# Kernel optimization log

Hardware: AMD Instinct MI355X
Metric: run time of the kernel (lower is better)

The kernel has to match this reference:

```python
import jax, jax.numpy as jnp
import numpy as np

B, S, D = 4, 2048, 1024
LAYERS = 2
NLOPS = 4
GAMMA = 0.01          # lindblad_gamma
COND_TH = 100.0       # condition_threshold
EPS = 1e-6


def setup_inputs() -> dict:
    key = jax.random.key(0)
    ks = jax.random.split(key, 9)
    x_real = jax.random.normal(ks[0], (B, S, D), jnp.float32)
    x_imag = jax.random.normal(ks[1], (B, S, D), jnp.float32)
    H_prev = jax.random.uniform(ks[2], (B, D, D), jnp.float32)
    eye = jnp.eye(D, dtype=jnp.float32)
    # base mixing layer (stand-in for ComplexMamba3Layer): near-identity complex linear
    W_real = eye[None, :, :] + 0.02 * jax.random.normal(ks[3], (LAYERS, D, D), jnp.float32)
    W_imag = 0.02 * jax.random.normal(ks[4], (LAYERS, D, D), jnp.float32)
    L_ops = 0.5 * jax.random.normal(ks[5], (LAYERS, NLOPS, D), jnp.float32)
    theta = jax.random.uniform(ks[6], (LAYERS,), jnp.float32, 0.0, 0.5)
    jump_scale = 0.9 * jnp.ones((LAYERS,), jnp.float32)
    kappa_th = 0.1 * jnp.ones((LAYERS,), jnp.float32)   # curvature_threshold per layer
    return dict(x_real=x_real, x_imag=x_imag, H_prev=H_prev,
                W_real=W_real, W_imag=W_imag, L_ops=L_ops,
                theta=theta, jump_scale=jump_scale, kappa_th=kappa_th)


def _v8_forward(x_real, x_imag, H_prev, W_real, W_imag, L_ops, theta, jump_scale, kappa_th):
    psi = jax.lax.complex(x_real, x_imag)  # [B,S,D] complex64
    Hp = H_prev                            # [B,D,D] real (prev Hamiltonian, detached)
    for l in range(LAYERS):
        residual = psi
        # --- base layer: complex linear mix ---
        Wc = jax.lax.complex(W_real[l], W_imag[l])
        out = jnp.einsum('bsd,de->bse', psi, Wc)
        branch_delta = out - residual
        # --- delta-RMS normalize (no_grad -> stop_gradient) ---
        rms = jnp.sqrt(jnp.clip(jnp.mean(branch_delta.real ** 2 + branch_delta.imag ** 2), 1e-12, None))
        rms = jax.lax.stop_gradient(jnp.maximum(rms, 1e-3))
        b = branch_delta / rms
        # --- Lindblad dissipation: diagonal damping gamma * sum_k L_k^2 ---
        damp = GAMMA * jnp.sum(L_ops[l] ** 2, axis=0)  # [D]
        b = b * (1.0 - damp)
        # --- approximate Hamiltonian H = (1/S) sum_s |psi_s><psi_s| (no_grad) ---
        mag = jnp.abs(b)                                # [B,S,D]
        H = jax.lax.stop_gradient(jnp.einsum('bsd,bse->bde', mag, mag) / S)  # [B,D,D]
        # --- hybrid automata: curvature K = ||H - Hp||_F / ||Hp||_F ---
        diff_n = jnp.sqrt(jnp.sum((H - Hp) ** 2, axis=(1, 2)))
        prev_n = jnp.sqrt(jnp.sum(Hp ** 2, axis=(1, 2)))
        K = diff_n / (prev_n + EPS)                     # [B]
        jumped = K > kappa_th[l]
        b = jnp.where(jumped[:, None, None], b * jump_scale[l].astype(jnp.complex64), b)
        Hp = H
        # --- quaternionic escape: diag-based condition estimate, phase rotation ---
        dg = jnp.diagonal(H, axis1=1, axis2=2)          # [B,D]
        cond = jnp.max(dg, axis=1) / (jnp.min(dg, axis=1) + 1e-12)
        escaped = cond > COND_TH
        rot = jnp.exp(1j * theta[l]).astype(jnp.complex64)
        b = jnp.where(escaped[:, None, None], b * rot, b)
        # --- rescale and residual ---
        b = b * rms
        psi = residual + b
    return jnp.stack([psi.real, psi.imag], axis=0)  # [2,B,S,D] float32


def reference(x_real, x_imag, H_prev, W_real, W_imag, L_ops, theta, jump_scale, kappa_th):
    return _v8_forward(x_real, x_imag, H_prev, W_real, W_imag, L_ops, theta, jump_scale, kappa_th)
```

## Files before the change

kernel.cpp:

```cpp
#include <hip/hip_runtime.h>

#define B_ 4
#define S_ 2048
#define D_ 1024
#define M_ (B_*S_)
#define K2_ 2048
#define N2_ 2048
#define NTOT (B_*S_*D_)
#define DD (D_*D_)

typedef __attribute__((ext_vector_type(4))) float f32x4;
typedef __attribute__((ext_vector_type(8))) short short8;
typedef __attribute__((ext_vector_type(4))) unsigned short u16x4;
typedef __attribute__((ext_vector_type(8))) unsigned short u16x8;

static __device__ __forceinline__ unsigned short f2bf(float f) {
    union { float f; unsigned int u; } v; v.f = f;
    unsigned int u = v.u;
    unsigned int r = (u + 0x7fffu + ((u >> 16) & 1u)) >> 16;
    return (unsigned short)r;
}
static __device__ __forceinline__ float bf2f(unsigned short h) {
    union { unsigned int u; float f; } v; v.u = ((unsigned int)h) << 16;
    return v.f;
}


__global__ __launch_bounds__(256, 2) void gemm_main2(const unsigned short* __restrict__ A2,
                                                     const unsigned short* __restrict__ B2T,
                                                     unsigned short* __restrict__ bd2,
                                                     unsigned short* __restrict__ magT,
                                                     float* __restrict__ scal, int l)
{
    __shared__ unsigned short smem[3 * 128 * 64];
    __shared__ float red[4];
    unsigned short* As  = smem;
    unsigned short* Bsr = smem + 8192;
    unsigned short* Bsi = smem + 16384;

    f32x4 accr[4][4], acci[4][4];
#pragma unroll
    for (int i = 0; i < 4; ++i)
#pragma unroll
        for (int j = 0; j < 4; ++j) { accr[i][j] = (f32x4)0.0f; acci[i][j] = (f32x4)0.0f; }

    const int nt = blockIdx.x, mt = blockIdx.y;
    const int tid = threadIdx.x, wave = tid >> 6, lane = tid & 63;
    const int q = lane >> 4, lm = lane & 15;
    const int wm = (wave >> 1) * 64, wn = (wave & 1) * 64;
    const int crow = lane >> 3;
    const int gcol = ((lane & 7) ^ crow) * 8;

    const unsigned short* Ag  = A2  + (long)mt * 128 * K2_;
    const unsigned short* Bgr = B2T + (long)(nt * 128) * K2_;
    const unsigned short* Bgi = B2T + (long)(nt * 128 + 1024) * K2_;

    for (int kt = 0; kt < K2_ / 64; ++kt) {
        const long k0 = (long)kt * 64;
        __syncthreads();
#pragma unroll
        for (int i2 = 0; i2 < 4; ++i2) {
            int c   = i2 * 4 + wave;
            int row = c * 8 + crow;
            long go = (long)row * K2_ + k0 + gcol;
            __builtin_amdgcn_global_load_lds((const __attribute__((address_space(1))) void*)(Ag + go),
                                             (__attribute__((address_space(3))) void*)(As + c * 512), 16, 0, 0);
            __builtin_amdgcn_global_load_lds((const __attribute__((address_space(1))) void*)(Bgr + go),
                                             (__attribute__((address_space(3))) void*)(Bsr + c * 512), 16, 0, 0);
            __builtin_amdgcn_global_load_lds((const __attribute__((address_space(1))) void*)(Bgi + go),
                                             (__attribute__((address_space(3))) void*)(Bsi + c * 512), 16, 0, 0);
        }
        __syncthreads();
#pragma unroll
        for (int kk = 0; kk < 64; kk += 32) {
            short8 a[4], br[4], bi[4];
#pragma unroll
            for (int t = 0; t < 4; ++t) {
                int arow  = wm + t * 16 + lm;
                int aslot = ((kk >> 3) + q) ^ (arow & 7);
                a[t] = *(const short8*)(As + arow * 64 + aslot * 8);
                int brow  = wn + t * 16 + lm;
                int bslot = ((kk >> 3) + q) ^ (brow & 7);
                br[t] = *(const short8*)(Bsr + brow * 64 + bslot * 8);
                bi[t] = *(const short8*)(Bsi + brow * 64 + bslot * 8);
            }
#pragma unroll
            for (int um = 0; um < 4; ++um)
#pragma unroll
                for (int un = 0; un < 4; ++un) {
                    accr[um][un] = __builtin_amdgcn_mfma_f32_16x16x32_bf16(a[um], br[un], accr[um][un], 0, 0, 0);
                    acci[um][un] = __builtin_amdgcn_mfma_f32_16x16x32_bf16(a[um], bi[un], acci[um][un], 0, 0, 0);
                }
        }
    }

    __syncthreads();
    unsigned short* magLds = smem;
    float ss = 0.f;
#pragma unroll
    for (int um = 0; um < 4; ++um) {
#pragma unroll
        for (int un = 0; un < 4; ++un) {
            int colb = wn + un * 16 + lm;
            int coln = nt * 128 + colb;
            u16x4 magv;
#pragma unroll
            for (int i = 0; i < 4; ++i) {
                long rowm = (long)mt * 128 + wm + um * 16 + q * 4 + i;
                float vr = accr[um][un][i];
                float vi = acci[um][un][i];
                bd2[rowm * N2_ + coln]        = f2bf(vr);
                bd2[rowm * N2_ + 1024 + coln] = f2bf(vi);
                float s2 = vr * vr + vi * vi;
                ss += s2;
                magv[i] = f2bf(sqrtf(s2));
            }
            *(u16x4*)(magLds + colb * 136 + wm + um * 16 + q * 4) = magv;
        }
    }
    for (int off = 32; off > 0; off >>= 1) ss += __shfl_down(ss, off);
    if (lane == 0) red[wave] = ss;
    __syncthreads();
    if (tid == 0) atomicAdd(scal + l, red[0] + red[1] + red[2] + red[3]);

    const int b   = mt >> 4;
    const long s0 = (long)(mt & 15) * 128;
#pragma unroll
    for (int it = 0; it < 8; ++it) {
        int sid = it * 256 + tid;
        int row = sid >> 4, seg = sid & 15;
        unsigned short* dst = magT + (long)b * D_ * S_ + (long)(nt * 128 + row) * S_ + s0 + seg * 8;
        *(u16x8*)dst = *(const u16x8*)(magLds + row * 136 + seg * 8);
    }
}

__device__ __forceinline__ void mfma_gemm_64(const unsigned short* __restrict__ Ag, long astride,
                                             const unsigned short* __restrict__ Bg, long bstride,
                                             int kiters,
                                             unsigned short* As, unsigned short* Bs,
                                             f32x4 acc[2][2])
{
    const int tid  = threadIdx.x;
    const int wave = tid >> 6, lane = tid & 63;
    const int q    = lane >> 4, lm = lane & 15;
    const int wm   = (wave >> 1) * 32, wn = (wave & 1) * 32;
    const int crow = lane >> 3;
    const int gcol = ((lane & 7) ^ crow) * 8;

    for (int kt = 0; kt < kiters; ++kt) {
        const long k0 = (long)kt * 64;
        __syncthreads();
#pragma unroll
        for (int i2 = 0; i2 < 2; ++i2) {
            int c   = i2 * 4 + wave;
            int row = c * 8 + crow;
            const unsigned short* ga = Ag + (long)row * astride + k0 + gcol;
            const unsigned short* gb = Bg + (long)row * bstride + k0 + gcol;
            __builtin_amdgcn_global_load_lds((const __attribute__((address_space(1))) void*)ga,
                                             (__attribute__((address_space(3))) void*)(As + c * 512), 16, 0, 0);
            __builtin_amdgcn_global_load_lds((const __attribute__((address_space(1))) void*)gb,
                                             (__attribute__((address_space(3))) void*)(Bs + c * 512), 16, 0, 0);
        }
        __syncthreads();
#pragma unroll
        for (int kk = 0; kk < 64; kk += 32) {
            short8 a[2], b[2];
#pragma unroll
            for (int t = 0; t < 2; ++t) {
                int arow  = wm + t * 16 + lm;
                int aslot = ((kk >> 3) + q) ^ (arow & 7);
                a[t] = *(const short8*)(As + arow * 64 + aslot * 8);
                int brow  = wn + t * 16 + lm;
                int bslot = ((kk >> 3) + q) ^ (brow & 7);
                b[t] = *(const short8*)(Bs + brow * 64 + bslot * 8);
            }
#pragma unroll
            for (int um = 0; um < 2; ++um)
#pragma unroll
                for (int un = 0; un < 2; ++un)
                    acc[um][un] = __builtin_amdgcn_mfma_f32_16x16x32_bf16(a[um], b[un], acc[um][un], 0, 0, 0);
        }
    }
}

__global__ __launch_bounds__(256) void gemm_H(const unsigned short* __restrict__ magT,
                                              const float* __restrict__ Hp,
                                              float* __restrict__ H,
                                              float* __restrict__ scal,
                                              const float* __restrict__ dampv, int l)
{
    __shared__ unsigned short As[64 * 64];
    __shared__ unsigned short Bs[64 * 64];
    __shared__ float redd[4], redp[4];

    int idx = blockIdx.x, ty = 0;
    while (idx >= 16 - ty) { idx -= 16 - ty; ++ty; }
    const int tx = ty + idx;
    const int b = blockIdx.y;
    const int diag = (tx == ty);

    f32x4 acc[2][2];
#pragma unroll
    for (int i = 0; i < 2; ++i)
#pragma unroll
        for (int j = 0; j < 2; ++j) acc[i][j] = (f32x4)0.0f;

    const unsigned short* Mb = magT + (long)b * D_ * S_;
    mfma_gemm_64(Mb + (long)ty * 64 * S_, S_,
                 Mb + (long)tx * 64 * S_, S_, S_ / 64, As, Bs, acc);

    float mean = fmaxf(scal[l] / (float)NTOT, 1e-12f);
    float inv  = 1.0f / fmaxf(sqrtf(mean), 1e-3f);
    const float scale = inv * inv / (float)S_;

    const int tid = threadIdx.x, wave = tid >> 6, lane = tid & 63;
    const int q = lane >> 4, lm = lane & 15;
    const int wm = (wave >> 1) * 32, wn = (wave & 1) * 32;
    float d2 = 0.f, p2 = 0.f;
#pragma unroll
    for (int um = 0; um < 2; ++um) {
#pragma unroll
        for (int un = 0; un < 2; ++un) {
            int coln = tx * 64 + wn + un * 16 + lm;
            float de = dampv[coln];
#pragma unroll
            for (int i = 0; i < 4; ++i) {
                int rowm = ty * 64 + wm + um * 16 + q * 4 + i;
                float h = acc[um][un][i] * scale * dampv[rowm] * de;
                long adr = (long)b * DD + (long)rowm * D_ + coln;
                float hp1 = Hp[adr];
                float df1 = h - hp1;
                if (diag) {
                    H[adr] = h;
                    d2 += df1 * df1;
                    p2 += hp1 * hp1;
                    if (rowm == coln) {
                        atomicMax((int*)scal + 18 + l * 4 + b, __float_as_int(h));
                        atomicMin((int*)scal + 26 + l * 4 + b, __float_as_int(h));
                    }
                } else {
                    long adrT = (long)b * DD + (long)coln * D_ + rowm;
                    float hp2 = Hp[adrT];
                    H[adr]  = h;
                    H[adrT] = h;
                    float df2 = h - hp2;
                    d2 += df1 * df1 + df2 * df2;
                    p2 += hp1 * hp1 + hp2 * hp2;
                }
            }
        }
    }
    for (int off = 32; off > 0; off >>= 1) { d2 += __shfl_down(d2, off); p2 += __shfl_down(p2, off); }
    if (lane == 0) { redd[wave] = d2; redp[wave] = p2; }
    __syncthreads();
    if (tid == 0) {
        atomicAdd(scal + 2 + l * 4 + b,  redd[0] + redd[1] + redd[2] + redd[3]);
        atomicAdd(scal + 10 + l * 4 + b, redp[0] + redp[1] + redp[2] + redp[3]);
    }
}

__global__ void init_kernel(const float* __restrict__ xr, const float* __restrict__ xi,
                            float* __restrict__ psi_r, float* __restrict__ psi_i,
                            unsigned short* __restrict__ A2, float* __restrict__ scal)
{
    if (blockIdx.x == 0 && threadIdx.x < 34)
        scal[threadIdx.x] = (threadIdx.x >= 26) ? 3.402823466e38f : 0.0f;
    long t = (long)blockIdx.x * 256 + threadIdx.x;
    long i = t * 4;
    f32x4 r  = *(const f32x4*)(xr + i);
    f32x4 im = *(const f32x4*)(xi + i);
    *(f32x4*)(psi_r + i) = r;
    *(f32x4*)(psi_i + i) = im;
    long m = i / D_; int d = (int)(i % D_);
    u16x4 rr, ii;
#pragma unroll
    for (int j = 0; j < 4; ++j) { rr[j] = f2bf(r[j]); ii[j] = f2bf(im[j]); }
    *(u16x4*)(A2 + m * K2_ + d) = rr;
    *(u16x4*)(A2 + m * K2_ + D_ + d) = ii;
}

__global__ __launch_bounds__(256) void pack_b2t(const float* __restrict__ Wr_all,
                                                const float* __restrict__ Wi_all,
                                                unsigned short* __restrict__ B2T, int l)
{
    __shared__ float T[64][65];
    const float* Wr = Wr_all + (long)l * DD;
    const float* Wi = Wi_all + (long)l * DD;
    int k0 = blockIdx.x * 64;
    int n0 = blockIdx.y * 64;
    int t = threadIdx.x;
#pragma unroll
    for (int it = 0; it < 16; ++it) {
        int idx = it * 256 + t;
        int kl = idx >> 6, nl = idx & 63;
        int k = k0 + kl, n = n0 + nl;
        float v;
        if (k < D_) v = (n < D_) ? Wr[k * D_ + n] : Wi[k * D_ + (n - D_)];
        else        v = (n < D_) ? -Wi[(k - D_) * D_ + n] : Wr[(k - D_) * D_ + (n - D_)];
        if (k == n) v -= 1.0f;
        T[kl][nl] = v;
    }
    __syncthreads();
#pragma unroll
    for (int it = 0; it < 16; ++it) {
        int idx = it * 256 + t;
        int nl = idx >> 6, kl = idx & 63;
        B2T[(long)(n0 + nl) * K2_ + (k0 + kl)] = f2bf(T[kl][nl]);
    }
}

__global__ void damp_kernel(const float* __restrict__ Lops, float* __restrict__ dampv)
{
    int g = blockIdx.x;
    int l = g >> 2;
    int d = (g & 3) * 256 + threadIdx.x;
    const float* Lp = Lops + (long)l * 4 * D_;
    float s = 0.f;
#pragma unroll
    for (int k = 0; k < 4; ++k) { float v = Lp[k * D_ + d]; s += v * v; }
    dampv[l * D_ + d] = 1.0f - 0.01f * s;
}

__global__ void update_kernel(const unsigned short* __restrict__ bd2,
                              const float* __restrict__ dampv,
                              const float* __restrict__ scal,
                              const float* __restrict__ theta,
                              const float* __restrict__ jscale,
                              const float* __restrict__ kappa, int l,
                              float* __restrict__ psi_r,
                              float* __restrict__ psi_i,
                              unsigned short* __restrict__ A2,
                              int write_a2)
{
    long t = (long)blockIdx.x * 256 + threadIdx.x;
    long i = t * 4;
    long m = i / D_; int d = (int)(i % D_);
    int b = (int)(m >> 11);

    float dn = sqrtf(scal[2 + l * 4 + b]);
    float pn = sqrtf(scal[10 + l * 4 + b]);
    float K  = dn / (pn + 1e-6f);
    float mx = __int_as_float(((const int*)scal)[18 + l * 4 + b]);
    float mn = __int_as_float(((const int*)scal)[26 + l * 4 + b]);
    int jumped  = K > kappa[l];
    int escaped = (mx / (mn + 1e-12f)) > 100.0f;
    float js = jumped ? jscale[l] : 1.0f;
    float th = theta[l];
    float fr = js * (escaped ? cosf(th) : 1.0f);
    float fi = js * (escaped ? sinf(th) : 0.0f);

    u16x4 brv = *(const u16x4*)(bd2 + m * N2_ + d);
    u16x4 biv = *(const u16x4*)(bd2 + m * N2_ + D_ + d);
    f32x4 w  = *(const f32x4*)(dampv + d);
    f32x4 pr = *(const f32x4*)(psi_r + i);
    f32x4 pi = *(const f32x4*)(psi_i + i);
    u16x4 ar, ai;
#pragma unroll
    for (int j = 0; j < 4; ++j) {
        float br = bf2f(brv[j]) * w[j];
        float bi = bf2f(biv[j]) * w[j];
        float nr = pr[j] + br * fr - bi * fi;
        float ni = pi[j] + br * fi + bi * fr;
        pr[j] = nr; pi[j] = ni;
        ar[j] = f2bf(nr); ai[j] = f2bf(ni);
    }
    *(f32x4*)(psi_r + i) = pr;
    *(f32x4*)(psi_i + i) = pi;
    if (write_a2) {
        *(u16x4*)(A2 + m * K2_ + d) = ar;
        *(u16x4*)(A2 + m * K2_ + D_ + d) = ai;
    }
}

extern "C" void kernel_launch(void* const* d_in, const int* in_sizes, int n_in,
                              void* d_out, int out_size, void* d_ws, size_t ws_size,
                              hipStream_t stream)
{
    const float* xr     = (const float*)d_in[0];
    const float* xi     = (const float*)d_in[1];
    const float* Hprev  = (const float*)d_in[2];
    const float* Wr     = (const float*)d_in[3];
    const float* Wi     = (const float*)d_in[4];
    const float* Lops   = (const float*)d_in[5];
    const float* theta  = (const float*)d_in[6];
    const float* jscale = (const float*)d_in[7];
    const float* kappa  = (const float*)d_in[8];

    float* psi_r = (float*)d_out;
    float* psi_i = psi_r + NTOT;

    char* ws = (char*)d_ws;
    unsigned short* A2   = (unsigned short*)ws;
    unsigned short* B2T  = (unsigned short*)(ws + 33554432);
    unsigned short* bd2  = (unsigned short*)(ws + 41943040);
    unsigned short* magT = (unsigned short*)(ws + 75497472);
    float* H             = (float*)(ws + 92274688);
    float* scal          = (float*)(ws + 109051904);
    float* dampv         = scal + 64;

    init_kernel<<<NTOT / 4 / 256, 256, 0, stream>>>(xr, xi, psi_r, psi_i, A2, scal);
    damp_kernel<<<8, 256, 0, stream>>>(Lops, dampv);

    for (int l = 0; l < 2; ++l) {
        const float* Hp = (l == 0) ? Hprev : H;
        pack_b2t<<<dim3(32, 32), 256, 0, stream>>>(Wr, Wi, B2T, l);
        gemm_main2<<<dim3(8, M_ / 128), 256, 0, stream>>>(A2, B2T, bd2, magT, scal, l);
        gemm_H<<<dim3(136, B_), 256, 0, stream>>>(magT, Hp, H, scal, dampv + l * D_, l);
        update_kernel<<<NTOT / 4 / 256, 256, 0, stream>>>(
            bd2, dampv + l * D_, scal, theta, jscale, kappa, l,
            psi_r, psi_i, A2, l == 0);
    }
}
```

Before: 457.5 us.

## Split-K the Hamiltonian GEMM with 128x128 tiles plus separate reduce kernel

After: 487.5 us. 6.6% more time.

```diff
diff --git a/kernel.cpp b/kernel.cpp
--- a/kernel.cpp
+++ b/kernel.cpp
@@ -134,16 +134,16 @@
     }
 }
 
-__device__ __forceinline__ void mfma_gemm_64(const unsigned short* __restrict__ Ag, long astride,
-                                             const unsigned short* __restrict__ Bg, long bstride,
-                                             int kiters,
-                                             unsigned short* As, unsigned short* Bs,
-                                             f32x4 acc[2][2])
+__device__ __forceinline__ void mfma_gemm_128(const unsigned short* __restrict__ Ag, long astride,
+                                              const unsigned short* __restrict__ Bg, long bstride,
+                                              int kiters,
+                                              unsigned short* As, unsigned short* Bs,
+                                              f32x4 acc[4][4])
 {
     const int tid  = threadIdx.x;
     const int wave = tid >> 6, lane = tid & 63;
     const int q    = lane >> 4, lm = lane & 15;
-    const int wm   = (wave >> 1) * 32, wn = (wave & 1) * 32;
+    const int wm   = (wave >> 1) * 64, wn = (wave & 1) * 64;
     const int crow = lane >> 3;
     const int gcol = ((lane & 7) ^ crow) * 8;
 
@@ -151,7 +151,7 @@
         const long k0 = (long)kt * 64;
         __syncthreads();
 #pragma unroll
-        for (int i2 = 0; i2 < 2; ++i2) {
+        for (int i2 = 0; i2 < 4; ++i2) {
             int c   = i2 * 4 + wave;
             int row = c * 8 + crow;
             const unsigned short* ga = Ag + (long)row * astride + k0 + gcol;
@@ -164,9 +164,9 @@
         __syncthreads();
 #pragma unroll
         for (int kk = 0; kk < 64; kk += 32) {
-            short8 a[2], b[2];
-#pragma unroll
-            for (int t = 0; t < 2; ++t) {
+            short8 a[4], b[4];
+#pragma unroll
+            for (int t = 0; t < 4; ++t) {
                 int arow  = wm + t * 16 + lm;
                 int aslot = ((kk >> 3) + q) ^ (arow & 7);
                 a[t] = *(const short8*)(As + arow * 64 + aslot * 8);
@@ -175,83 +175,109 @@
                 b[t] = *(const short8*)(Bs + brow * 64 + bslot * 8);
             }
 #pragma unroll
-            for (int um = 0; um < 2; ++um)
-#pragma unroll
-                for (int un = 0; un < 2; ++un)
+            for (int um = 0; um < 4; ++um)
+#pragma unroll
+                for (int un = 0; un < 4; ++un)
                     acc[um][un] = __builtin_amdgcn_mfma_f32_16x16x32_bf16(a[um], b[un], acc[um][un], 0, 0, 0);
         }
     }
 }
 
-__global__ __launch_bounds__(256) void gemm_H(const unsigned short* __restrict__ magT,
-                                              const float* __restrict__ Hp,
-                                              float* __restrict__ H,
-                                              float* __restrict__ scal,
-                                              const float* __restrict__ dampv, int l)
-{
-    __shared__ unsigned short As[64 * 64];
-    __shared__ unsigned short Bs[64 * 64];
+__global__ __launch_bounds__(256, 2) void gemmH_split(const unsigned short* __restrict__ magT,
+                                                      float* __restrict__ pbuf)
+{
+    __shared__ unsigned short As[128 * 64];
+    __shared__ unsigned short Bs[128 * 64];
+    f32x4 acc[4][4];
+#pragma unroll
+    for (int i = 0; i < 4; ++i)
+#pragma unroll
+        for (int j = 0; j < 4; ++j) acc[i][j] = (f32x4)0.0f;
+
+    const int pair = blockIdx.x, b = blockIdx.y, kc = blockIdx.z;
+    int idx = pair, ty = 0;
+    while (idx >= 8 - ty) { idx -= 8 - ty; ++ty; }
+    const int tx = ty + idx;
+
+    const unsigned short* Mb = magT + (long)b * D_ * S_ + (long)kc * 512;
+    mfma_gemm_128(Mb + (long)ty * 128 * S_, S_,
+                  Mb + (long)tx * 128 * S_, S_, 8, As, Bs, acc);
+
+    float* pt = pbuf + ((long)(kc * 36 + pair) * B_ + b) * 16384;
+    const int tid = threadIdx.x, wave = tid >> 6, lane = tid & 63;
+    const int q = lane >> 4, lm = lane & 15;
+    const int wm = (wave >> 1) * 64, wn = (wave & 1) * 64;
+#pragma unroll
+    for (int um = 0; um < 4; ++um)
+#pragma unroll
+        for (int un = 0; un < 4; ++un) {
+            int c = wn + un * 16 + lm;
+#pragma unroll
+            for (int i = 0; i < 4; ++i) {
+                int r = wm + um * 16 + q * 4 + i;
+                pt[r * 128 + c] = acc[um][un][i];
+            }
+        }
+}
+
+__global__ __launch_bounds__(256) void reduce_H(const float* __restrict__ pbuf,
+                                                const float* __restrict__ Hp,
+                                                float* __restrict__ H,
+                                                float* __restrict__ scal,
+                                                const float* __restrict__ dampv, int l)
+{
     __shared__ float redd[4], redp[4];
-
-    int idx = blockIdx.x, ty = 0;
-    while (idx >= 16 - ty) { idx -= 16 - ty; ++ty; }
-    const int tx = ty + idx;
-    const int b = blockIdx.y;
-    const int diag = (tx == ty);
-
-    f32x4 acc[2][2];
-#pragma unroll
-    for (int i = 0; i < 2; ++i)
-#pragma unroll
-        for (int j = 0; j < 2; ++j) acc[i][j] = (f32x4)0.0f;
-
-    const unsigned short* Mb = magT + (long)b * D_ * S_;
-    mfma_gemm_64(Mb + (long)ty * 64 * S_, S_,
-                 Mb + (long)tx * 64 * S_, S_, S_ / 64, As, Bs, acc);
+    const int pair = blockIdx.x, b = blockIdx.y;
+    int idx0 = pair, ty = 0;
+    while (idx0 >= 8 - ty) { idx0 -= 8 - ty; ++ty; }
+    const int tx = ty + idx0;
+    const int diag_tile = (tx == ty);
 
     float mean = fmaxf(scal[l] / (float)NTOT, 1e-12f);
     float inv  = 1.0f / fmaxf(sqrtf(mean), 1e-3f);
     const float scale = inv * inv / (float)S_;
 
-    const int tid = threadIdx.x, wave = tid >> 6, lane = tid & 63;
-    const int q = lane >> 4, lm = lane & 15;
-    const int wm = (wave >> 1) * 32, wn = (wave & 1) * 32;
+    const int tid = threadIdx.x;
     float d2 = 0.f, p2 = 0.f;
-#pragma unroll
-    for (int um = 0; um < 2; ++um) {
-#pragma unroll
-        for (int un = 0; un < 2; ++un) {
-            int coln = tx * 64 + wn + un * 16 + lm;
-            float de = dampv[coln];
-#pragma unroll
-            for (int i = 0; i < 4; ++i) {
-                int rowm = ty * 64 + wm + um * 16 + q * 4 + i;
-                float h = acc[um][un][i] * scale * dampv[rowm] * de;
-                long adr = (long)b * DD + (long)rowm * D_ + coln;
-                float hp1 = Hp[adr];
-                float df1 = h - hp1;
-                if (diag) {
-                    H[adr] = h;
-                    d2 += df1 * df1;
-                    p2 += hp1 * hp1;
-                    if (rowm == coln) {
-                        atomicMax((int*)scal + 18 + l * 4 + b, __float_as_int(h));
-                        atomicMin((int*)scal + 26 + l * 4 + b, __float_as_int(h));
-                    }
-                } else {
-                    long adrT = (long)b * DD + (long)coln * D_ + rowm;
-                    float hp2 = Hp[adrT];
-                    H[adr]  = h;
-                    H[adrT] = h;
-                    float df2 = h - hp2;
-                    d2 += df1 * df1 + df2 * df2;
-                    p2 += hp1 * hp1 + hp2 * hp2;
-                }
+    float dmx = 0.f, dmn = 3.402823466e38f;
+    for (int it = 0; it < 64; ++it) {
+        int idx = it * 256 + tid;
+        int r = idx >> 7, c = idx & 127;
+        int gr = ty * 128 + r, gc = tx * 128 + c;
+        float s = pbuf[((long)(0 * 36 + pair) * B_ + b) * 16384 + idx]
+                + pbuf[((long)(1 * 36 + pair) * B_ + b) * 16384 + idx]
+                + pbuf[((long)(2 * 36 + pair) * B_ + b) * 16384 + idx]
+                + pbuf[((long)(3 * 36 + pair) * B_ + b) * 16384 + idx];
+        float h = s * scale * dampv[gr] * dampv[gc];
+        long adr = (long)b * DD + (long)gr * D_ + gc;
+        if (l == 0) {
+            float hp1 = Hp[adr];
+            H[adr] = h;
+            float df1 = h - hp1;
+            if (diag_tile) {
+                d2 += df1 * df1; p2 += hp1 * hp1;
+            } else {
+                float hp2 = Hp[(long)b * DD + (long)gc * D_ + gr];
+                float df2 = h - hp2;
+                d2 += df1 * df1 + df2 * df2;
+                p2 += hp1 * hp1 + hp2 * hp2;
             }
-        }
-    }
+        } else {
+            float hp1 = Hp[adr];
+            float df1 = h - hp1;
+            float w = diag_tile ? 1.0f : 2.0f;
+            d2 += w * df1 * df1;
+            p2 += w * hp1 * hp1;
+        }
+        if (diag_tile && gr == gc) { dmx = fmaxf(dmx, h); dmn = fminf(dmn, h); }
+    }
+    int lane = tid & 63, wave = tid >> 6;
     for (int off = 32; off > 0; off >>= 1) { d2 += __shfl_down(d2, off); p2 += __shfl_down(p2, off); }
     if (lane == 0) { redd[wave] = d2; redp[wave] = p2; }
+    if (diag_tile) {
+        atomicMax((int*)scal + 18 + l * 4 + b, __float_as_int(dmx));
+        atomicMin((int*)scal + 26 + l * 4 + b, __float_as_int(dmn));
+    }
     __syncthreads();
     if (tid == 0) {
         atomicAdd(scal + 2 + l * 4 + b,  redd[0] + redd[1] + redd[2] + redd[3]);
@@ -260,7 +286,6 @@
 }
 
 __global__ void init_kernel(const float* __restrict__ xr, const float* __restrict__ xi,
-                            float* __restrict__ psi_r, float* __restrict__ psi_i,
                             unsigned short* __restrict__ A2, float* __restrict__ scal)
 {
     if (blockIdx.x == 0 && threadIdx.x < 34)
@@ -269,8 +294,6 @@
     long i = t * 4;
     f32x4 r  = *(const f32x4*)(xr + i);
     f32x4 im = *(const f32x4*)(xi + i);
-    *(f32x4*)(psi_r + i) = r;
-    *(f32x4*)(psi_i + i) = im;
     long m = i / D_; int d = (int)(i % D_);
     u16x4 rr, ii;
 #pragma unroll
@@ -327,8 +350,10 @@
                               const float* __restrict__ theta,
                               const float* __restrict__ jscale,
                               const float* __restrict__ kappa, int l,
-                              float* __restrict__ psi_r,
-                              float* __restrict__ psi_i,
+                              const float* __restrict__ src_r,
+                              const float* __restrict__ src_i,
+                              float* __restrict__ dst_r,
+                              float* __restrict__ dst_i,
                               unsigned short* __restrict__ A2,
                               int write_a2)
 {
@@ -352,8 +377,8 @@
     u16x4 brv = *(const u16x4*)(bd2 + m * N2_ + d);
     u16x4 biv = *(const u16x4*)(bd2 + m * N2_ + D_ + d);
     f32x4 w  = *(const f32x4*)(dampv + d);
-    f32x4 pr = *(const f32x4*)(psi_r + i);
-    f32x4 pi = *(const f32x4*)(psi_i + i);
+    f32x4 pr = *(const f32x4*)(src_r + i);
+    f32x4 pi = *(const f32x4*)(src_i + i);
     u16x4 ar, ai;
 #pragma unroll
     for (int j = 0; j < 4; ++j) {
@@ -364,8 +389,8 @@
         pr[j] = nr; pi[j] = ni;
         ar[j] = f2bf(nr); ai[j] = f2bf(ni);
     }
-    *(f32x4*)(psi_r + i) = pr;
-    *(f32x4*)(psi_i + i) = pi;
+    *(f32x4*)(dst_r + i) = pr;
+    *(f32x4*)(dst_i + i) = pi;
     if (write_a2) {
         *(u16x4*)(A2 + m * K2_ + d) = ar;
         *(u16x4*)(A2 + m * K2_ + D_ + d) = ai;
@@ -391,6 +416,7 @@
 
     char* ws = (char*)d_ws;
     unsigned short* A2   = (unsigned short*)ws;
+    float* pbuf          = (float*)ws;
     unsigned short* B2T  = (unsigned short*)(ws + 33554432);
     unsigned short* bd2  = (unsigned short*)(ws + 41943040);
     unsigned short* magT = (unsigned short*)(ws + 75497472);
@@ -398,16 +424,18 @@
     float* scal          = (float*)(ws + 109051904);
     float* dampv         = scal + 64;
 
-    init_kernel<<<NTOT / 4 / 256, 256, 0, stream>>>(xr, xi, psi_r, psi_i, A2, scal);
+    init_kernel<<<NTOT / 4 / 256, 256, 0, stream>>>(xr, xi, A2, scal);
     damp_kernel<<<8, 256, 0, stream>>>(Lops, dampv);
 
     for (int l = 0; l < 2; ++l) {
-        const float* Hp = (l == 0) ? Hprev : H;
         pack_b2t<<<dim3(32, 32), 256, 0, stream>>>(Wr, Wi, B2T, l);
         gemm_main2<<<dim3(8, M_ / 128), 256, 0, stream>>>(A2, B2T, bd2, magT, scal, l);
-        gemm_H<<<dim3(136, B_), 256, 0, stream>>>(magT, Hp, H, scal, dampv + l * D_, l);
+        gemmH_split<<<dim3(36, B_, 4), 256, 0, stream>>>(magT, pbuf);
+        reduce_H<<<dim3(36, B_), 256, 0, stream>>>(
+            pbuf, (l == 0) ? Hprev : H, H, scal, dampv + l * D_, l);
         update_kernel<<<NTOT / 4 / 256, 256, 0, stream>>>(
             bd2, dampv + l * D_, scal, theta, jscale, kappa, l,
+            (l == 0) ? xr : psi_r, (l == 0) ? xi : psi_i,
             psi_r, psi_i, A2, l == 0);
     }
 }
```

## Trim psi and H traffic, widen gemm_H K-step, and reduce diagonal atomics

Applied to the files above, without the earlier changes.

Result: faster. 427.9 us (-6.5%).

```diff
diff --git a/kernel.cpp b/kernel.cpp
--- a/kernel.cpp
+++ b/kernel.cpp
@@ -134,89 +134,85 @@
     }
 }
 
-__device__ __forceinline__ void mfma_gemm_64(const unsigned short* __restrict__ Ag, long astride,
-                                             const unsigned short* __restrict__ Bg, long bstride,
-                                             int kiters,
-                                             unsigned short* As, unsigned short* Bs,
-                                             f32x4 acc[2][2])
-{
-    const int tid  = threadIdx.x;
-    const int wave = tid >> 6, lane = tid & 63;
-    const int q    = lane >> 4, lm = lane & 15;
-    const int wm   = (wave >> 1) * 32, wn = (wave & 1) * 32;
+__global__ __launch_bounds__(256, 4) void gemm_H(const unsigned short* __restrict__ magT,
+                                                 const float* __restrict__ Hp,
+                                                 float* __restrict__ H,
+                                                 float* __restrict__ scal,
+                                                 const float* __restrict__ dampv, int l)
+{
+    __shared__ unsigned short As[2 * 64 * 64];
+    __shared__ unsigned short Bs[2 * 64 * 64];
+    __shared__ float redd[4], redp[4];
+
+    const int slot = blockIdx.x;
+    const int b = slot & 3;
+    int pair = (slot >> 2) * 68 + blockIdx.y;
+    int idx = pair, ty = 0;
+    while (idx >= 16 - ty) { idx -= 16 - ty; ++ty; }
+    const int tx = ty + idx;
+    const int diag = (tx == ty);
+
+    f32x4 acc[2][2];
+#pragma unroll
+    for (int i = 0; i < 2; ++i)
+#pragma unroll
+        for (int j = 0; j < 2; ++j) acc[i][j] = (f32x4)0.0f;
+
+    const int tid = threadIdx.x, wave = tid >> 6, lane = tid & 63;
+    const int q = lane >> 4, lm = lane & 15;
+    const int wm = (wave >> 1) * 32, wn = (wave & 1) * 32;
     const int crow = lane >> 3;
     const int gcol = ((lane & 7) ^ crow) * 8;
 
-    for (int kt = 0; kt < kiters; ++kt) {
-        const long k0 = (long)kt * 64;
+    const unsigned short* Ag = magT + (long)b * D_ * S_ + (long)ty * 64 * S_;
+    const unsigned short* Bg = magT + (long)b * D_ * S_ + (long)tx * 64 * S_;
+
+    for (int kt = 0; kt < 16; ++kt) {
+        const long k0 = (long)kt * 128;
         __syncthreads();
 #pragma unroll
-        for (int i2 = 0; i2 < 2; ++i2) {
-            int c   = i2 * 4 + wave;
-            int row = c * 8 + crow;
-            const unsigned short* ga = Ag + (long)row * astride + k0 + gcol;
-            const unsigned short* gb = Bg + (long)row * bstride + k0 + gcol;
-            __builtin_amdgcn_global_load_lds((const __attribute__((address_space(1))) void*)ga,
-                                             (__attribute__((address_space(3))) void*)(As + c * 512), 16, 0, 0);
-            __builtin_amdgcn_global_load_lds((const __attribute__((address_space(1))) void*)gb,
-                                             (__attribute__((address_space(3))) void*)(Bs + c * 512), 16, 0, 0);
+        for (int p = 0; p < 2; ++p) {
+#pragma unroll
+            for (int i2 = 0; i2 < 2; ++i2) {
+                int c   = i2 * 4 + wave;
+                int row = c * 8 + crow;
+                long go = (long)row * S_ + k0 + p * 64 + gcol;
+                __builtin_amdgcn_global_load_lds((const __attribute__((address_space(1))) void*)(Ag + go),
+                                                 (__attribute__((address_space(3))) void*)(As + p * 4096 + c * 512), 16, 0, 0);
+                __builtin_amdgcn_global_load_lds((const __attribute__((address_space(1))) void*)(Bg + go),
+                                                 (__attribute__((address_space(3))) void*)(Bs + p * 4096 + c * 512), 16, 0, 0);
+            }
         }
         __syncthreads();
 #pragma unroll
-        for (int kk = 0; kk < 64; kk += 32) {
-            short8 a[2], b[2];
-#pragma unroll
-            for (int t = 0; t < 2; ++t) {
-                int arow  = wm + t * 16 + lm;
-                int aslot = ((kk >> 3) + q) ^ (arow & 7);
-                a[t] = *(const short8*)(As + arow * 64 + aslot * 8);
-                int brow  = wn + t * 16 + lm;
-                int bslot = ((kk >> 3) + q) ^ (brow & 7);
-                b[t] = *(const short8*)(Bs + brow * 64 + bslot * 8);
+        for (int p = 0; p < 2; ++p) {
+#pragma unroll
+            for (int kk = 0; kk < 64; kk += 32) {
+                short8 a[2], bb[2];
+#pragma unroll
+                for (int t = 0; t < 2; ++t) {
+                    int arow  = wm + t * 16 + lm;
+                    int aslot = ((kk >> 3) + q) ^ (arow & 7);
+                    a[t] = *(const short8*)(As + p * 4096 + arow * 64 + aslot * 8);
+                    int brow  = wn + t * 16 + lm;
+                    int bslot = ((kk >> 3) + q) ^ (brow & 7);
+                    bb[t] = *(const short8*)(Bs + p * 4096 + brow * 64 + bslot * 8);
+                }
+#pragma unroll
+                for (int um = 0; um < 2; ++um)
+#pragma unroll
+                    for (int un = 0; un < 2; ++un)
+                        acc[um][un] = __builtin_amdgcn_mfma_f32_16x16x32_bf16(a[um], bb[un], acc[um][un], 0, 0, 0);
             }
-#pragma unroll
-            for (int um = 0; um < 2; ++um)
-#pragma unroll
-                for (int un = 0; un < 2; ++un)
-                    acc[um][un] = __builtin_amdgcn_mfma_f32_16x16x32_bf16(a[um], b[un], acc[um][un], 0, 0, 0);
-        }
-    }
-}
-
-__global__ __launch_bounds__(256) void gemm_H(const unsigned short* __restrict__ magT,
-                                              const float* __restrict__ Hp,
-                                              float* __restrict__ H,
-                                              float* __restrict__ scal,
-                                              const float* __restrict__ dampv, int l)
-{
-    __shared__ unsigned short As[64 * 64];
-    __shared__ unsigned short Bs[64 * 64];
-    __shared__ float redd[4], redp[4];
-
-    int idx = blockIdx.x, ty = 0;
-    while (idx >= 16 - ty) { idx -= 16 - ty; ++ty; }
-    const int tx = ty + idx;
-    const int b = blockIdx.y;
-    const int diag = (tx == ty);
-
-    f32x4 acc[2][2];
-#pragma unroll
-    for (int i = 0; i < 2; ++i)
-#pragma unroll
-        for (int j = 0; j < 2; ++j) acc[i][j] = (f32x4)0.0f;
-
-    const unsigned short* Mb = magT + (long)b * D_ * S_;
-    mfma_gemm_64(Mb + (long)ty * 64 * S_, S_,
-                 Mb + (long)tx * 64 * S_, S_, S_ / 64, As, Bs, acc);
+        }
+    }
 
     float mean = fmaxf(scal[l] / (float)NTOT, 1e-12f);
     float inv  = 1.0f / fmaxf(sqrtf(mean), 1e-3f);
     const float scale = inv * inv / (float)S_;
 
-    const int tid = threadIdx.x, wave = tid >> 6, lane = tid & 63;
-    const int q = lane >> 4, lm = lane & 15;
-    const int wm = (wave >> 1) * 32, wn = (wave & 1) * 32;
     float d2 = 0.f, p2 = 0.f;
+    float dmx = 0.f, dmn = 3.402823466e38f;
 #pragma unroll
     for (int um = 0; um < 2; ++um) {
 #pragma unroll
@@ -231,18 +227,14 @@
                 float hp1 = Hp[adr];
                 float df1 = h - hp1;
                 if (diag) {
-                    H[adr] = h;
+                    if (l == 0) H[adr] = h;
                     d2 += df1 * df1;
                     p2 += hp1 * hp1;
-                    if (rowm == coln) {
-                        atomicMax((int*)scal + 18 + l * 4 + b, __float_as_int(h));
-                        atomicMin((int*)scal + 26 + l * 4 + b, __float_as_int(h));
-                    }
+                    if (rowm == coln) { dmx = fmaxf(dmx, h); dmn = fminf(dmn, h); }
                 } else {
                     long adrT = (long)b * DD + (long)coln * D_ + rowm;
                     float hp2 = Hp[adrT];
-                    H[adr]  = h;
-                    H[adrT] = h;
+                    if (l == 0) { H[adr] = h; H[adrT] = h; }
                     float df2 = h - hp2;
                     d2 += df1 * df1 + df2 * df2;
                     p2 += hp1 * hp1 + hp2 * hp2;
@@ -252,6 +244,16 @@
     }
     for (int off = 32; off > 0; off >>= 1) { d2 += __shfl_down(d2, off); p2 += __shfl_down(p2, off); }
     if (lane == 0) { redd[wave] = d2; redp[wave] = p2; }
+    if (diag) {
+        for (int off = 32; off > 0; off >>= 1) {
+            dmx = fmaxf(dmx, __shfl_down(dmx, off));
+            dmn = fminf(dmn, __shfl_down(dmn, off));
+        }
+        if (lm == 0) {
+            atomicMax((int*)scal + 18 + l * 4 + b, __float_as_int(dmx));
+            atomicMin((int*)scal + 26 + l * 4 + b, __float_as_int(dmn));
+        }
+    }
     __syncthreads();
     if (tid == 0) {
         atomicAdd(scal + 2 + l * 4 + b,  redd[0] + redd[1] + redd[2] + redd[3]);
@@ -260,7 +262,6 @@
 }
 
 __global__ void init_kernel(const float* __restrict__ xr, const float* __restrict__ xi,
-                            float* __restrict__ psi_r, float* __restrict__ psi_i,
                             unsigned short* __restrict__ A2, float* __restrict__ scal)
 {
     if (blockIdx.x == 0 && threadIdx.x < 34)
@@ -269,8 +270,6 @@
     long i = t * 4;
     f32x4 r  = *(const f32x4*)(xr + i);
     f32x4 im = *(const f32x4*)(xi + i);
-    *(f32x4*)(psi_r + i) = r;
-    *(f32x4*)(psi_i + i) = im;
     long m = i / D_; int d = (int)(i % D_);
     u16x4 rr, ii;
 #pragma unroll
@@ -327,8 +326,10 @@
                               const float* __restrict__ theta,
                               const float* __restrict__ jscale,
                               const float* __restrict__ kappa, int l,
-                              float* __restrict__ psi_r,
-                              float* __restrict__ psi_i,
+                              const float* __restrict__ src_r,
+                              const float* __restrict__ src_i,
+                              float* __restrict__ dst_r,
+                              float* __restrict__ dst_i,
                               unsigned short* __restrict__ A2,
                               int write_a2)
 {
@@ -352,8 +353,8 @@
     u16x4 brv = *(const u16x4*)(bd2 + m * N2_ + d);
     u16x4 biv = *(const u16x4*)(bd2 + m * N2_ + D_ + d);
     f32x4 w  = *(const f32x4*)(dampv + d);
-    f32x4 pr = *(const f32x4*)(psi_r + i);
-    f32x4 pi = *(const f32x4*)(psi_i + i);
+    f32x4 pr = *(const f32x4*)(src_r + i);
+    f32x4 pi = *(const f32x4*)(src_i + i);
     u16x4 ar, ai;
 #pragma unroll
     for (int j = 0; j < 4; ++j) {
@@ -364,8 +365,8 @@
         pr[j] = nr; pi[j] = ni;
         ar[j] = f2bf(nr); ai[j] = f2bf(ni);
     }
-    *(f32x4*)(psi_r + i) = pr;
-    *(f32x4*)(psi_i + i) = pi;
+    *(f32x4*)(dst_r + i) = pr;
+    *(f32x4*)(dst_i + i) = pi;
     if (write_a2) {
         *(u16x4*)(A2 + m * K2_ + d) = ar;
         *(u16x4*)(A2 + m * K2_ + D_ + d) = ai;
@@ -398,16 +399,20 @@
     float* scal          = (float*)(ws + 109051904);
     float* dampv         = scal + 64;
 
-    init_kernel<<<NTOT / 4 / 256, 256, 0, stream>>>(xr, xi, psi_r, psi_i, A2, scal);
+    init_kernel<<<NTOT / 4 / 256, 256, 0, stream>>>(xr, xi, A2, scal);
     damp_kernel<<<8, 256, 0, stream>>>(Lops, dampv);
 
-    for (int l = 0; l < 2; ++l) {
-        const float* Hp = (l == 0) ? Hprev : H;
-        pack_b2t<<<dim3(32, 32), 256, 0, stream>>>(Wr, Wi, B2T, l);
-        gemm_main2<<<dim3(8, M_ / 128), 256, 0, stream>>>(A2, B2T, bd2, magT, scal, l);
-        gemm_H<<<dim3(136, B_), 256, 0, stream>>>(magT, Hp, H, scal, dampv + l * D_, l);
-        update_kernel<<<NTOT / 4 / 256, 256, 0, stream>>>(
-            bd2, dampv + l * D_, scal, theta, jscale, kappa, l,
-            psi_r, psi_i, A2, l == 0);
-    }
-}
+    pack_b2t<<<dim3(32, 32), 256, 0, stream>>>(Wr, Wi, B2T, 0);
+    gemm_main2<<<dim3(8, M_ / 128), 256, 0, stream>>>(A2, B2T, bd2, magT, scal, 0);
+    gemm_H<<<dim3(8, 68), 256, 0, stream>>>(magT, Hprev, H, scal, dampv, 0);
+    update_kernel<<<NTOT / 4 / 256, 256, 0, stream>>>(
+        bd2, dampv, scal, theta, jscale, kappa, 0,
+        xr, xi, psi_r, psi_i, A2, 1);
+
+    pack_b2t<<<dim3(32, 32), 256, 0, stream>>>(Wr, Wi, B2T, 1);
+    gemm_main2<<<dim3(8, M_ / 128), 256, 0, stream>>>(A2, B2T, bd2, magT, scal, 1);
+    gemm_H<<<dim3(8, 68), 256, 0, stream>>>(magT, H, H, scal, dampv + D_, 1);
+    update_kernel<<<NTOT / 4 / 256, 256, 0, stream>>>(
+        bd2, dampv + D_, scal, theta, jscale, kappa, 1,
+        psi_r, psi_i, psi_r, psi_i, (unsigned short*)nullptr, 0);
+}
```
